# Performance work log

Hardware: AMD Instinct MI355X
Metric: run time of the kernel (lower is better)

Reference implementation:

```python
import jax, jax.numpy as jnp
import numpy as np

WD, WH, WW = 1, 8, 8           # window size
NH = 2                          # num heads
EPS = 1e-5                      # torch LayerNorm default


def _layernorm(x, g, b):
    mu = jnp.mean(x, axis=-1, keepdims=True)
    var = jnp.mean((x - mu) ** 2, axis=-1, keepdims=True)
    return (x - mu) * jax.lax.rsqrt(var + EPS) * g + b


def setup_inputs() -> dict:
    key = jax.random.key(0)
    ks = jax.random.split(key, 12)
    C, H = 192, 768  # dim, mlp hidden
    w = lambda k, shape: (jax.random.normal(k, shape, jnp.float32) * 0.02)
    return {
        "x": jax.random.normal(ks[0], (2, 8, 96, 96, C), jnp.float32),
        "norm3_g": jnp.ones((C,), jnp.float32),
        "norm3_b": jnp.zeros((C,), jnp.float32),
        "in_proj_w": w(ks[1], (3 * C, C)),
        "in_proj_b": jnp.zeros((3 * C,), jnp.float32),
        "out_proj_w": w(ks[2], (C, C)),
        "out_proj_b": jnp.zeros((C,), jnp.float32),
        "norm4_g": jnp.ones((C,), jnp.float32),
        "norm4_b": jnp.zeros((C,), jnp.float32),
        "fc1_w": w(ks[3], (H, C)),
        "fc1_b": jnp.zeros((H,), jnp.float32),
        "fc2_w": w(ks[4], (C, H)),
        "fc2_b": jnp.zeros((C,), jnp.float32),
    }


def _part3(x, norm3_g, norm3_b, in_proj_w, in_proj_b, out_proj_w, out_proj_b):
    B, D, H, W, C = x.shape
    Dn, Hn, Wn = D // WD, H // WH, W // WW
    P = Hn * Wn          # spatial windows
    Wt = WD * WH * WW    # tokens per window (64)
    L = Dn * Wt          # attention sequence length

    xn = _layernorm(x, norm3_g, norm3_b)
    # window partition: (B, Dn, Hn, Wn, wd, wh, ww, C)
    xw = xn.reshape(B, Dn, WD, Hn, WH, Wn, WW, C).transpose(0, 1, 3, 5, 2, 4, 6, 7)
    # tgt: (B, Dn, P, Wt, C) -> h: (B*P, Dn*Wt, C)
    tgt = xw.reshape(B, Dn, P, Wt, C)
    h = tgt.transpose(0, 2, 1, 3, 4).reshape(B * P, L, C)

    # qkv projection (torch Linear convention: x @ W.T + b)
    qkv = h @ in_proj_w.T + in_proj_b          # (Bp, L, 3C)
    q, k, v = jnp.split(qkv, 3, axis=-1)
    hd = C // NH
    q = q.reshape(B * P, L, NH, hd)
    k = k.reshape(B * P, L, NH, hd)
    v = v.reshape(B * P, L, NH, hd)

    # block-causal mask over temporal index (each block is Wt x Wt)
    neg_inf = jnp.finfo(jnp.float32).min
    tmask = jnp.triu(jnp.full((Dn, Dn), neg_inf, jnp.float32), k=1)
    mask = jnp.repeat(jnp.repeat(tmask, Wt, axis=0), Wt, axis=1)  # (L, L)

    scale = 1.0 / np.sqrt(hd)
    scores = jnp.einsum("blhd,bmhd->bhlm", q * scale, k) + mask
    attn = jax.nn.softmax(scores, axis=-1)
    out = jnp.einsum("bhlm,bmhd->blhd", attn, v).reshape(B * P, L, C)
    out = out @ out_proj_w.T + out_proj_b

    # reverse: (B, P, Dn, Wt, C) -> windows -> (B, D, H, W, C)
    out = out.reshape(B, P, Dn, Wt, C).transpose(0, 2, 1, 3, 4)
    out = out.reshape(B, Dn, Hn, Wn, WD, WH, WW, C)
    out = out.transpose(0, 1, 4, 2, 5, 3, 6, 7).reshape(B, D, H, W, C)
    return out


def reference(x, norm3_g, norm3_b, in_proj_w, in_proj_b, out_proj_w, out_proj_b,
              norm4_g, norm4_b, fc1_w, fc1_b, fc2_w, fc2_b):
    x = x + _part3(x, norm3_g, norm3_b, in_proj_w, in_proj_b, out_proj_w, out_proj_b)
    xn = _layernorm(x, norm4_g, norm4_b)
    mlp = jax.nn.gelu(xn @ fc1_w.T + fc1_b, approximate=False) @ fc2_w.T + fc2_b
    return x + mlp
```

## Files before the change

### kernel.cpp

```cpp
#include <hip/hip_runtime.h>
#include <cstdint>
#include <cstddef>


typedef float   f32x4  __attribute__((ext_vector_type(4)));
typedef __bf16  bf16x8 __attribute__((ext_vector_type(8)));
typedef unsigned int   u32x4  __attribute__((ext_vector_type(4)));
typedef unsigned short u16x4  __attribute__((ext_vector_type(4)));

#define DEVI __device__ __forceinline__

DEVI float bf2f(unsigned short u) {
    union { unsigned int i; float f; } v; v.i = ((unsigned int)u) << 16; return v.f;
}
DEVI unsigned short f2bf(float f) {
    unsigned int u = __builtin_bit_cast(unsigned int, f);
    unsigned int r = u + 0x7fffu + ((u >> 16) & 1u);
    return (unsigned short)(r >> 16);
}
DEVI float gelu_fast(float v) {
    float t = v * v;
    float z = v * (1.5957691216057308f + 0.07135481627f * t);
    float e = __expf(z);
    float r = 2.0f / (1.0f + e);
    return v - 0.5f * v * r;
}

typedef __attribute__((address_space(3))) unsigned char       lds_u8;
typedef __attribute__((address_space(1))) const unsigned char g_u8;
DEVI void gl_lds16(const void* g, void* l) {
    __builtin_amdgcn_global_load_lds((g_u8*)g, (lds_u8*)l, 16, 0, 0);
}

__global__ __launch_bounds__(256) void k_wconv(const float* __restrict__ wqkv,
                                               const float* __restrict__ wout,
                                               const float* __restrict__ wfc1,
                                               const float* __restrict__ wfc2,
                                               unsigned short* __restrict__ oq,
                                               unsigned short* __restrict__ oo,
                                               unsigned short* __restrict__ o1,
                                               unsigned short* __restrict__ o2) {
    int i = blockIdx.x * 256 + threadIdx.x;
    if (i < 122880) {
        int r = i / 192;
        oq[i] = (r < 576) ? f2bf(wqkv[i]) : (unsigned short)0;
    } else if (i < 172032) {
        int j = i - 122880; int r = j / 192;
        oo[j] = (r < 192) ? f2bf(wout[j]) : (unsigned short)0;
    } else if (i < 319488) {
        int j = i - 172032;
        o1[j] = f2bf(wfc1[j]);
    } else if (i < 516096) {
        int j = i - 319488; int r = j / 768;
        o2[j] = (r < 192) ? f2bf(wfc2[j]) : (unsigned short)0;
    }
}

__global__ __launch_bounds__(256) void k_ln3(const float* __restrict__ x,
                                             const float* __restrict__ g,
                                             const float* __restrict__ bsh,
                                             unsigned short* __restrict__ h) {
    int w = threadIdx.x >> 6, lane = threadIdx.x & 63;
    int token = blockIdx.x * 4 + w;
    const float* xp = x + (size_t)token * 192;
    float v0 = xp[lane], v1 = xp[lane + 64], v2 = xp[lane + 128];
    float s = v0 + v1 + v2;
#pragma unroll
    for (int off = 32; off; off >>= 1) s += __shfl_xor(s, off);
    float mean = s * (1.f / 192.f);
    float d0 = v0 - mean, d1 = v1 - mean, d2 = v2 - mean;
    float q = d0 * d0 + d1 * d1 + d2 * d2;
#pragma unroll
    for (int off = 32; off; off >>= 1) q += __shfl_xor(q, off);
    float rs = rsqrtf(q * (1.f / 192.f) + 1e-5f);
    int b  = token / (8 * 96 * 96);
    int r0 = token - b * (8 * 96 * 96);
    int d  = r0 / (96 * 96);
    int r1 = r0 - d * (96 * 96);
    int hh = r1 / 96;
    int ww = r1 - hh * 96;
    int bp = b * 144 + (hh >> 3) * 12 + (ww >> 3);
    int l  = d * 64 + (hh & 7) * 8 + (ww & 7);
    unsigned short* hp = h + ((size_t)bp * 512 + l) * 192;
    hp[lane]       = f2bf(d0 * rs * g[lane]       + bsh[lane]);
    hp[lane + 64]  = f2bf(d1 * rs * g[lane + 64]  + bsh[lane + 64]);
    hp[lane + 128] = f2bf(d2 * rs * g[lane + 128] + bsh[lane + 128]);
}

__global__ __launch_bounds__(256) void k_ln4b(const unsigned short* __restrict__ yb,
                                              const float* __restrict__ g,
                                              const float* __restrict__ bsh,
                                              unsigned short* __restrict__ xn) {
    int sub = threadIdx.x >> 5, tl = threadIdx.x & 31;
    size_t row = (size_t)blockIdx.x * 8 + sub;
    const unsigned int* rp = reinterpret_cast<const unsigned int*>(yb + row * 192);
    float v[6];
#pragma unroll
    for (int j = 0; j < 3; j++) {
        unsigned int w = rp[tl + 32 * j];
        v[2 * j]     = bf2f((unsigned short)(w & 0xffffu));
        v[2 * j + 1] = bf2f((unsigned short)(w >> 16));
    }
    float s = v[0] + v[1] + v[2] + v[3] + v[4] + v[5];
#pragma unroll
    for (int off = 1; off < 32; off <<= 1) s += __shfl_xor(s, off);
    float mean = s * (1.f / 192.f);
    float q = 0.f;
#pragma unroll
    for (int j = 0; j < 6; j++) { v[j] -= mean; q += v[j] * v[j]; }
#pragma unroll
    for (int off = 1; off < 32; off <<= 1) q += __shfl_xor(q, off);
    float rs = rsqrtf(q * (1.f / 192.f) + 1e-5f);
    unsigned int* op = reinterpret_cast<unsigned int*>(xn + row * 192);
#pragma unroll
    for (int j = 0; j < 3; j++) {
        int c = (tl + 32 * j) * 2;
        unsigned short lo = f2bf(v[2 * j]     * rs * g[c]     + bsh[c]);
        unsigned short hi = f2bf(v[2 * j + 1] * rs * g[c + 1] + bsh[c + 1]);
        op[tl + 32 * j] = ((unsigned int)hi << 16) | lo;
    }
}

template <int EPI, int K, int NF>
__global__ __launch_bounds__(256) void k_gemm128(const unsigned short* __restrict__ A,
                                                 const unsigned short* __restrict__ Bw,
                                                 const float* __restrict__ bias,
                                                 unsigned short* __restrict__ outb,
                                                 unsigned short* __restrict__ vt,
                                                 float* __restrict__ outf,
                                                 const float* __restrict__ res,
                                                 const unsigned short* __restrict__ resb) {
    constexpr int BN = NF * 32;
    __shared__ unsigned short As[2][128 * 64];
    __shared__ unsigned short Bs[2][BN * 64];
    const int tid = threadIdx.x;
    const int nwg = gridDim.x * gridDim.y;
    const int flat = blockIdx.y * gridDim.x + blockIdx.x;
    const int swz = (flat & 7) * (nwg >> 3) + (flat >> 3);
    const int bx = swz % gridDim.x, by = swz / gridDim.x;
    const int row0 = by * 128, col0 = bx * BN;
    const int wv = tid >> 6, lane = tid & 63, lr = lane & 15, lg = lane >> 4;
    const int wr = wv >> 1, wc = wv & 1;
    const int sr = lane >> 3, sc = lane & 7;
    f32x4 acc[4][NF] = {};

    auto stage = [&](int t, int buf) {
        int k0 = t * 64;
#pragma unroll
        for (int i = 0; i < 4; i++) {
            int gq = wv * 4 + i;
            int r = gq * 8 + sr;
            int j = sc ^ (r & 7);
            gl_lds16(A + (size_t)(row0 + r) * K + k0 + j * 8, &As[buf][gq * 512]);
        }
#pragma unroll
        for (int i = 0; i < NF; i++) {
            int gq = wv * NF + i;
            int r = gq * 8 + sr;
            int j = sc ^ (r & 7);
            gl_lds16(Bw + (size_t)(col0 + r) * K + k0 + j * 8, &Bs[buf][gq * 512]);
        }
    };

    const int NT = K / 64;
    stage(0, 0);
    for (int t = 0; t < NT; ++t) {
        int cur = t & 1;
        if (t + 1 < NT) {
            stage(t + 1, cur ^ 1);
            if constexpr (NF == 4) asm volatile("s_waitcnt vmcnt(8)" ::: "memory");
            else                   asm volatile("s_waitcnt vmcnt(10)" ::: "memory");
        } else {
            asm volatile("s_waitcnt vmcnt(0)" ::: "memory");
        }
        __builtin_amdgcn_sched_barrier(0);
        __builtin_amdgcn_s_barrier();
        __builtin_amdgcn_sched_barrier(0);
#pragma unroll
        for (int kk = 0; kk < 64; kk += 32) {
            bf16x8 af[4], bf[NF];
#pragma unroll
            for (int m = 0; m < 4; m++) {
                int r = wr * 64 + m * 16 + lr;
                int j = ((kk >> 3) + lg) ^ (r & 7);
                af[m] = __builtin_bit_cast(bf16x8,
                    *reinterpret_cast<const u32x4*>(&As[cur][r * 64 + j * 8]));
            }
#pragma unroll
            for (int n = 0; n < NF; n++) {
                int r = wc * (NF * 16) + n * 16 + lr;
                int j = ((kk >> 3) + lg) ^ (r & 7);
                bf[n] = __builtin_bit_cast(bf16x8,
                    *reinterpret_cast<const u32x4*>(&Bs[cur][r * 64 + j * 8]));
            }
#pragma unroll
            for (int m = 0; m < 4; m++)
#pragma unroll
                for (int n = 0; n < NF; n++)
                    acc[m][n] = __builtin_amdgcn_mfma_f32_16x16x32_bf16(bf[n], af[m], acc[m][n], 0, 0, 0);
        }
        __builtin_amdgcn_sched_barrier(0);
        __builtin_amdgcn_s_barrier();
        __builtin_amdgcn_sched_barrier(0);
    }

#pragma unroll
    for (int m = 0; m < 4; m++) {
        const int arow = row0 + wr * 64 + m * 16 + lr;
#pragma unroll
        for (int n = 0; n < NF; n++) {
            const int colb = col0 + wc * (NF * 16) + n * 16 + lg * 4;
            if constexpr (EPI == 0) {
                if (colb < 384) {
                    f32x4 b4 = *reinterpret_cast<const f32x4*>(bias + colb);
                    float sc2 = (colb < 192) ? 0.1020620726159658f : 1.f;
                    u16x4 pk;
#pragma unroll
                    for (int rr = 0; rr < 4; rr++) pk[rr] = f2bf((acc[m][n][rr] + b4[rr]) * sc2);
                    *reinterpret_cast<u16x4*>(outb + (size_t)arow * 384 + colb) = pk;
                } else if (colb < 576) {
                    int head = (colb >= 480) ? 1 : 0;
                    int bp = arow >> 9, tok = arow & 511;
                    size_t vb = ((size_t)(bp * 2 + head) * 96 + (colb - 384 - head * 96)) * 512 + tok;
#pragma unroll
                    for (int rr = 0; rr < 4; rr++)
                        vt[vb + (size_t)rr * 512] = f2bf(acc[m][n][rr] + bias[colb + rr]);
                }
            } else if constexpr (EPI == 1) {
                if (colb < 192) {
                    int bp = arow >> 9, l = arow & 511;
                    int bb = bp / 144, p = bp - bb * 144;
                    int hn = p / 12, wn = p - hn * 12;
                    int dn = l >> 6, t_ = l & 63;
                    size_t tok = ((size_t)((bb * 8 + dn) * 96 + hn * 8 + (t_ >> 3)) * 96 + wn * 8 + (t_ & 7));
                    size_t idx = tok * 192 + colb;
                    f32x4 r4 = *reinterpret_cast<const f32x4*>(res + idx);
                    f32x4 b4 = *reinterpret_cast<const f32x4*>(bias + colb);
                    u16x4 pk;
#pragma unroll
                    for (int rr = 0; rr < 4; rr++) pk[rr] = f2bf(r4[rr] + acc[m][n][rr] + b4[rr]);
                    *reinterpret_cast<u16x4*>(outb + idx) = pk;
                }
            } else if constexpr (EPI == 2) {
                f32x4 b4 = *reinterpret_cast<const f32x4*>(bias + colb);
                u16x4 pk;
#pragma unroll
                for (int rr = 0; rr < 4; rr++) pk[rr] = f2bf(gelu_fast(acc[m][n][rr] + b4[rr]));
                *reinterpret_cast<u16x4*>(outb + (size_t)arow * 768 + colb) = pk;
            } else {
                f32x4 b4 = *reinterpret_cast<const f32x4*>(bias + colb);
                u16x4 rb = *reinterpret_cast<const u16x4*>(resb + (size_t)arow * 192 + colb);
                f32x4 o4;
#pragma unroll
                for (int rr = 0; rr < 4; rr++) o4[rr] = bf2f(rb[rr]) + acc[m][n][rr] + b4[rr];
                *reinterpret_cast<f32x4*>(outf + (size_t)arow * 192 + colb) = o4;
            }
        }
    }
}

__global__ __launch_bounds__(512) void k_attn(const unsigned short* __restrict__ qk,
                                              const unsigned short* __restrict__ vt,
                                              unsigned short* __restrict__ aout) {
    __shared__ unsigned short Ks[64][104];
    __shared__ unsigned short Vs[96][72];
    __shared__ unsigned short Ps[8][16][72];

    int bid = (blockIdx.x & 7) * 288 + (blockIdx.x >> 3);
    int bp = bid >> 3, rest = bid & 7, head = rest >> 2, pr = rest & 3;
    int tid = threadIdx.x, wv = tid >> 6, lane = tid & 63;
    int lr = lane & 15, lg = lane >> 4;
    int wq = wv & 3, wt = wv >> 2;
    int nk = 2 * pr + 2;

    size_t qrow0 = (size_t)bp * 512 + (size_t)(2 * pr + wt) * 64;
    const unsigned short* vbase = vt + (size_t)(bp * 2 + head) * 96 * 512;
    size_t krowb = (size_t)bp * 512;

    bf16x8 qf[3];
    {
        const unsigned short* qp = qk + (qrow0 + wq * 16 + lr) * 384 + head * 96 + lg * 8;
#pragma unroll
        for (int ks = 0; ks < 3; ks++)
            qf[ks] = __builtin_bit_cast(bf16x8, *reinterpret_cast<const u32x4*>(qp + ks * 32));
    }

    f32x4 o[6] = {};
    float m_ = -1e30f, lsum = 0.f;

    u32x4 sreg[3];
    auto issue = [&](int dnk) {
#pragma unroll
        for (int i = 0; i < 3; i++) {
            int c = tid + i * 512;
            if (c < 768) {
                int r = c / 12, cc = c - r * 12;
                sreg[i] = *reinterpret_cast<const u32x4*>(
                    qk + (krowb + dnk * 64 + r) * 384 + 192 + head * 96 + cc * 8);
            } else {
                int c2 = c - 768; int d = c2 >> 3, tb = c2 & 7;
                sreg[i] = *reinterpret_cast<const u32x4*>(
                    vbase + (size_t)d * 512 + dnk * 64 + tb * 8);
            }
        }
    };
    auto commit = [&]() {
#pragma unroll
        for (int i = 0; i < 3; i++) {
            int c = tid + i * 512;
            if (c < 768) {
                int r = c / 12, cc = c - r * 12;
                *reinterpret_cast<u32x4*>(&Ks[r][cc * 8]) = sreg[i];
            } else {
                int c2 = c - 768; int d = c2 >> 3, tb = c2 & 7;
                *reinterpret_cast<u32x4*>(&Vs[d][tb * 8]) = sreg[i];
            }
        }
    };

    issue(0);
    for (int dnk = 0; dnk < nk; ++dnk) {
        commit();
        __syncthreads();
        if (dnk + 1 < nk) issue(dnk + 1);
        if (wt == 1 || dnk < nk - 1) {
            f32x4 st[4] = {};
#pragma unroll
            for (int ks = 0; ks < 3; ks++) {
#pragma unroll
                for (int ct = 0; ct < 4; ct++) {
                    bf16x8 kf = __builtin_bit_cast(bf16x8,
                        *reinterpret_cast<const u32x4*>(&Ks[ct * 16 + lr][ks * 32 + lg * 8]));
                    st[ct] = __builtin_amdgcn_mfma_f32_16x16x32_bf16(kf, qf[ks], st[ct], 0, 0, 0);
                }
            }
            float mx = st[0][0];
#pragma unroll
            for (int ct = 0; ct < 4; ct++)
#pragma unroll
                for (int rr = 0; rr < 4; rr++) mx = fmaxf(mx, st[ct][rr]);
            mx = fmaxf(mx, __shfl_xor(mx, 16));
            mx = fmaxf(mx, __shfl_xor(mx, 32));
            float mnew = fmaxf(m_, mx);
            float corr = __expf(m_ - mnew);
            m_ = mnew;
            float ps = 0.f;
#pragma unroll
            for (int ct = 0; ct < 4; ct++) {
                u16x4 pk;
#pragma unroll
                for (int rr = 0; rr < 4; rr++) {
                    float pv = __expf(st[ct][rr] - mnew);
                    ps += pv;
                    pk[rr] = f2bf(pv);
                }
                *reinterpret_cast<u16x4*>(&Ps[wv][lr][ct * 16 + lg * 4]) = pk;
            }
            ps += __shfl_xor(ps, 16);
            ps += __shfl_xor(ps, 32);
            lsum = lsum * corr + ps;
#pragma unroll
            for (int rr = 0; rr < 4; rr++) {
                float cr = __shfl(corr, (lane & 48) | (lg * 4 + rr));
#pragma unroll
                for (int nf = 0; nf < 6; nf++) o[nf][rr] *= cr;
            }
#pragma unroll
            for (int kk = 0; kk < 2; kk++) {
                bf16x8 pf = __builtin_bit_cast(bf16x8,
                    *reinterpret_cast<const u32x4*>(&Ps[wv][lr][kk * 32 + lg * 8]));
#pragma unroll
                for (int nf = 0; nf < 6; nf++) {
                    bf16x8 vf = __builtin_bit_cast(bf16x8,
                        *reinterpret_cast<const u32x4*>(&Vs[nf * 16 + lr][kk * 32 + lg * 8]));
                    o[nf] = __builtin_amdgcn_mfma_f32_16x16x32_bf16(pf, vf, o[nf], 0, 0, 0);
                }
            }
        }
        __syncthreads();
    }

#pragma unroll
    for (int rr = 0; rr < 4; rr++) {
        float li = __shfl(lsum, (lane & 48) | (lg * 4 + rr));
        float inv = 1.f / li;
        size_t row = qrow0 + wq * 16 + lg * 4 + rr;
#pragma unroll
        for (int nf = 0; nf < 6; nf++)
            aout[row * 192 + head * 96 + nf * 16 + lr] = f2bf(o[nf][rr] * inv);
    }
}

extern "C" void kernel_launch(void* const* d_in, const int* in_sizes, int n_in,
                              void* d_out, int out_size, void* d_ws, size_t ws_size,
                              hipStream_t stream) {
    const float* x    = (const float*)d_in[0];
    const float* n3g  = (const float*)d_in[1];
    const float* n3b  = (const float*)d_in[2];
    const float* wqkv = (const float*)d_in[3];
    const float* bqkv = (const float*)d_in[4];
    const float* wout = (const float*)d_in[5];
    const float* bout = (const float*)d_in[6];
    const float* n4g  = (const float*)d_in[7];
    const float* n4b  = (const float*)d_in[8];
    const float* wfc1 = (const float*)d_in[9];
    const float* bfc1 = (const float*)d_in[10];
    const float* wfc2 = (const float*)d_in[11];
    const float* bfc2 = (const float*)d_in[12];
    float* out = (float*)d_out;

    char* ws = (char*)d_ws;
    unsigned short* qk     = (unsigned short*)(ws + 0);
    unsigned short* vt     = (unsigned short*)(ws + 113246208);
    unsigned short* h      = (unsigned short*)(ws + 169869312);
    unsigned short* attn   = (unsigned short*)(ws + 226492416);
    unsigned short* xn4    = (unsigned short*)(ws + 226492416);
    unsigned short* hidden = (unsigned short*)(ws + 0);
    unsigned short* wq_bf  = (unsigned short*)(ws + 283115520);
    unsigned short* wo_bf  = (unsigned short*)(ws + 283361280);
    unsigned short* w1_bf  = (unsigned short*)(ws + 283459584);
    unsigned short* w2_bf  = (unsigned short*)(ws + 283754496);
    unsigned short* ybf    = (unsigned short*)(ws + 284147712);

    k_wconv<<<2016, 256, 0, stream>>>(wqkv, wout, wfc1, wfc2, wq_bf, wo_bf, w1_bf, w2_bf);
    k_ln3<<<36864, 256, 0, stream>>>(x, n3g, n3b, h);
    k_gemm128<0, 192, 4><<<dim3(5, 1152), 256, 0, stream>>>(h, wq_bf, bqkv, qk, vt, nullptr, nullptr, nullptr);
    k_attn<<<2304, 512, 0, stream>>>(qk, vt, attn);
    k_gemm128<1, 192, 4><<<dim3(2, 1152), 256, 0, stream>>>(attn, wo_bf, bout, ybf, nullptr, nullptr, x, nullptr);
    k_ln4b<<<18432, 256, 0, stream>>>(ybf, n4g, n4b, xn4);
    k_gemm128<2, 192, 4><<<dim3(6, 1152), 256, 0, stream>>>(xn4, w1_bf, bfc1, hidden, nullptr, nullptr, nullptr, nullptr);
    k_gemm128<3, 768, 6><<<dim3(1, 1152), 256, 0, stream>>>(hidden, w2_bf, bfc2, nullptr, nullptr, out, nullptr, ybf);
}
```

Before: 600.5 us.

## Fuse LN4, fc1, GELU and fc2 into one MLP kernel; fold LN affine into weights

```diff
diff --git a/kernel.cpp b/kernel.cpp
--- a/kernel.cpp
+++ b/kernel.cpp
@@ -36,29 +36,49 @@
                                                const float* __restrict__ wout,
                                                const float* __restrict__ wfc1,
                                                const float* __restrict__ wfc2,
+                                               const float* __restrict__ n3g,
+                                               const float* __restrict__ n4g,
                                                unsigned short* __restrict__ oq,
                                                unsigned short* __restrict__ oo,
                                                unsigned short* __restrict__ o1,
                                                unsigned short* __restrict__ o2) {
     int i = blockIdx.x * 256 + threadIdx.x;
     if (i < 122880) {
-        int r = i / 192;
-        oq[i] = (r < 576) ? f2bf(wqkv[i]) : (unsigned short)0;
+        int r = i / 192, c = i - r * 192;
+        oq[i] = (r < 576) ? f2bf(wqkv[i] * n3g[c]) : (unsigned short)0;
     } else if (i < 172032) {
         int j = i - 122880; int r = j / 192;
         oo[j] = (r < 192) ? f2bf(wout[j]) : (unsigned short)0;
     } else if (i < 319488) {
-        int j = i - 172032;
-        o1[j] = f2bf(wfc1[j]);
+        int j = i - 172032; int c = j % 192;
+        o1[j] = f2bf(wfc1[j] * n4g[c]);
     } else if (i < 516096) {
         int j = i - 319488; int r = j / 768;
         o2[j] = (r < 192) ? f2bf(wfc2[j]) : (unsigned short)0;
     }
 }
 
+__global__ __launch_bounds__(256) void k_bias(const float* __restrict__ wqkv,
+                                              const float* __restrict__ bqkv,
+                                              const float* __restrict__ n3b,
+                                              const float* __restrict__ wfc1,
+                                              const float* __restrict__ bfc1,
+                                              const float* __restrict__ n4b,
+                                              float* __restrict__ beffq,
+                                              float* __restrict__ beff1) {
+    int wid = blockIdx.x * 4 + (threadIdx.x >> 6);
+    int lane = threadIdx.x & 63;
+    const float* wrow; const float* bb; float base; float* dst;
+    if (wid < 576) { wrow = wqkv + (size_t)wid * 192; bb = n3b; base = bqkv[wid]; dst = beffq + wid; }
+    else { int h = wid - 576; wrow = wfc1 + (size_t)h * 192; bb = n4b; base = bfc1[h]; dst = beff1 + h; }
+    float s = wrow[lane] * bb[lane] + wrow[lane + 64] * bb[lane + 64]
+            + wrow[lane + 128] * bb[lane + 128];
+#pragma unroll
+    for (int off = 32; off; off >>= 1) s += __shfl_xor(s, off);
+    if (lane == 0) *dst = base + s;
+}
+
 __global__ __launch_bounds__(256) void k_ln3(const float* __restrict__ x,
-                                             const float* __restrict__ g,
-                                             const float* __restrict__ bsh,
                                              unsigned short* __restrict__ h) {
     int w = threadIdx.x >> 6, lane = threadIdx.x & 63;
     int token = blockIdx.x * 4 + w;
@@ -82,43 +102,9 @@
     int bp = b * 144 + (hh >> 3) * 12 + (ww >> 3);
     int l  = d * 64 + (hh & 7) * 8 + (ww & 7);
     unsigned short* hp = h + ((size_t)bp * 512 + l) * 192;
-    hp[lane]       = f2bf(d0 * rs * g[lane]       + bsh[lane]);
-    hp[lane + 64]  = f2bf(d1 * rs * g[lane + 64]  + bsh[lane + 64]);
-    hp[lane + 128] = f2bf(d2 * rs * g[lane + 128] + bsh[lane + 128]);
-}
-
-__global__ __launch_bounds__(256) void k_ln4b(const unsigned short* __restrict__ yb,
-                                              const float* __restrict__ g,
-                                              const float* __restrict__ bsh,
-                                              unsigned short* __restrict__ xn) {
-    int sub = threadIdx.x >> 5, tl = threadIdx.x & 31;
-    size_t row = (size_t)blockIdx.x * 8 + sub;
-    const unsigned int* rp = reinterpret_cast<const unsigned int*>(yb + row * 192);
-    float v[6];
-#pragma unroll
-    for (int j = 0; j < 3; j++) {
-        unsigned int w = rp[tl + 32 * j];
-        v[2 * j]     = bf2f((unsigned short)(w & 0xffffu));
-        v[2 * j + 1] = bf2f((unsigned short)(w >> 16));
-    }
-    float s = v[0] + v[1] + v[2] + v[3] + v[4] + v[5];
-#pragma unroll
-    for (int off = 1; off < 32; off <<= 1) s += __shfl_xor(s, off);
-    float mean = s * (1.f / 192.f);
-    float q = 0.f;
-#pragma unroll
-    for (int j = 0; j < 6; j++) { v[j] -= mean; q += v[j] * v[j]; }
-#pragma unroll
-    for (int off = 1; off < 32; off <<= 1) q += __shfl_xor(q, off);
-    float rs = rsqrtf(q * (1.f / 192.f) + 1e-5f);
-    unsigned int* op = reinterpret_cast<unsigned int*>(xn + row * 192);
-#pragma unroll
-    for (int j = 0; j < 3; j++) {
-        int c = (tl + 32 * j) * 2;
-        unsigned short lo = f2bf(v[2 * j]     * rs * g[c]     + bsh[c]);
-        unsigned short hi = f2bf(v[2 * j + 1] * rs * g[c + 1] + bsh[c + 1]);
-        op[tl + 32 * j] = ((unsigned int)hi << 16) | lo;
-    }
+    hp[lane]       = f2bf(d0 * rs);
+    hp[lane + 64]  = f2bf(d1 * rs);
+    hp[lane + 128] = f2bf(d2 * rs);
 }
 
 template <int EPI, int K, int NF>
@@ -127,18 +113,15 @@
                                                  const float* __restrict__ bias,
                                                  unsigned short* __restrict__ outb,
                                                  unsigned short* __restrict__ vt,
-                                                 float* __restrict__ outf,
-                                                 const float* __restrict__ res,
-                                                 const unsigned short* __restrict__ resb) {
-    constexpr int BN = NF * 32;
+                                                 const float* __restrict__ res) {
     __shared__ unsigned short As[2][128 * 64];
-    __shared__ unsigned short Bs[2][BN * 64];
+    __shared__ unsigned short Bs[2][NF * 32 * 64];
     const int tid = threadIdx.x;
     const int nwg = gridDim.x * gridDim.y;
     const int flat = blockIdx.y * gridDim.x + blockIdx.x;
     const int swz = (flat & 7) * (nwg >> 3) + (flat >> 3);
     const int bx = swz % gridDim.x, by = swz / gridDim.x;
-    const int row0 = by * 128, col0 = bx * BN;
+    const int row0 = by * 128, col0 = bx * (NF * 32);
     const int wv = tid >> 6, lane = tid & 63, lr = lane & 15, lg = lane >> 4;
     const int wr = wv >> 1, wc = wv & 1;
     const int sr = lane >> 3, sc = lane & 7;
@@ -169,7 +152,7 @@
         if (t + 1 < NT) {
             stage(t + 1, cur ^ 1);
             if constexpr (NF == 4) asm volatile("s_waitcnt vmcnt(8)" ::: "memory");
-            else                   asm volatile("s_waitcnt vmcnt(10)" ::: "memory");
+            else                   asm volatile("s_waitcnt vmcnt(7)" ::: "memory");
         } else {
             asm volatile("s_waitcnt vmcnt(0)" ::: "memory");
         }
@@ -207,10 +190,10 @@
 #pragma unroll
     for (int m = 0; m < 4; m++) {
         const int arow = row0 + wr * 64 + m * 16 + lr;
-#pragma unroll
-        for (int n = 0; n < NF; n++) {
-            const int colb = col0 + wc * (NF * 16) + n * 16 + lg * 4;
-            if constexpr (EPI == 0) {
+        if constexpr (EPI == 0) {
+#pragma unroll
+            for (int n = 0; n < NF; n++) {
+                const int colb = col0 + wc * (NF * 16) + n * 16 + lg * 4;
                 if (colb < 384) {
                     f32x4 b4 = *reinterpret_cast<const f32x4*>(bias + colb);
                     float sc2 = (colb < 192) ? 0.1020620726159658f : 1.f;
@@ -226,34 +209,23 @@
                     for (int rr = 0; rr < 4; rr++)
                         vt[vb + (size_t)rr * 512] = f2bf(acc[m][n][rr] + bias[colb + rr]);
                 }
-            } else if constexpr (EPI == 1) {
-                if (colb < 192) {
-                    int bp = arow >> 9, l = arow & 511;
-                    int bb = bp / 144, p = bp - bb * 144;
-                    int hn = p / 12, wn = p - hn * 12;
-                    int dn = l >> 6, t_ = l & 63;
-                    size_t tok = ((size_t)((bb * 8 + dn) * 96 + hn * 8 + (t_ >> 3)) * 96 + wn * 8 + (t_ & 7));
-                    size_t idx = tok * 192 + colb;
-                    f32x4 r4 = *reinterpret_cast<const f32x4*>(res + idx);
-                    f32x4 b4 = *reinterpret_cast<const f32x4*>(bias + colb);
-                    u16x4 pk;
-#pragma unroll
-                    for (int rr = 0; rr < 4; rr++) pk[rr] = f2bf(r4[rr] + acc[m][n][rr] + b4[rr]);
-                    *reinterpret_cast<u16x4*>(outb + idx) = pk;
-                }
-            } else if constexpr (EPI == 2) {
+            }
+        } else {
+            int bp = arow >> 9, l = arow & 511;
+            int bb = bp / 144, p = bp - bb * 144;
+            int hn = p / 12, wn = p - hn * 12;
+            int dn = l >> 6, t_ = l & 63;
+            size_t tok = ((size_t)((bb * 8 + dn) * 96 + hn * 8 + (t_ >> 3)) * 96 + wn * 8 + (t_ & 7));
+#pragma unroll
+            for (int n = 0; n < NF; n++) {
+                const int colb = col0 + wc * (NF * 16) + n * 16 + lg * 4;
+                size_t idx = tok * 192 + colb;
+                f32x4 r4 = *reinterpret_cast<const f32x4*>(res + idx);
                 f32x4 b4 = *reinterpret_cast<const f32x4*>(bias + colb);
                 u16x4 pk;
 #pragma unroll
-                for (int rr = 0; rr < 4; rr++) pk[rr] = f2bf(gelu_fast(acc[m][n][rr] + b4[rr]));
-                *reinterpret_cast<u16x4*>(outb + (size_t)arow * 768 + colb) = pk;
-            } else {
-                f32x4 b4 = *reinterpret_cast<const f32x4*>(bias + colb);
-                u16x4 rb = *reinterpret_cast<const u16x4*>(resb + (size_t)arow * 192 + colb);
-                f32x4 o4;
-#pragma unroll
-                for (int rr = 0; rr < 4; rr++) o4[rr] = bf2f(rb[rr]) + acc[m][n][rr] + b4[rr];
-                *reinterpret_cast<f32x4*>(outf + (size_t)arow * 192 + colb) = o4;
+                for (int rr = 0; rr < 4; rr++) pk[rr] = f2bf(r4[rr] + acc[m][n][rr] + b4[rr]);
+                *reinterpret_cast<u16x4*>(outb + idx) = pk;
             }
         }
     }
@@ -388,6 +360,145 @@
 #pragma unroll
         for (int nf = 0; nf < 6; nf++)
             aout[row * 192 + head * 96 + nf * 16 + lr] = f2bf(o[nf][rr] * inv);
+    }
+}
+
+__global__ __launch_bounds__(256, 4) void k_mlp3(const unsigned short* __restrict__ ybf,
+                                                 const unsigned short* __restrict__ w1,
+                                                 const unsigned short* __restrict__ w2,
+                                                 const float* __restrict__ beff1,
+                                                 const float* __restrict__ b2,
+                                                 float* __restrict__ out) {
+    __shared__ unsigned short XN[3][64][64];
+    __shared__ unsigned short Hs[64][64];
+    const int tid = threadIdx.x;
+    const int bid = (blockIdx.x & 7) * 288 + (blockIdx.x >> 3);
+    const int row0 = bid * 64;
+    const int wv = tid >> 6, lane = tid & 63, lr = lane & 15, lg = lane >> 4;
+    const int tHalf = wv & 1, oH = wv >> 1;
+
+#pragma unroll
+    for (int i = 0; i < 6; i++) {
+        int g = wv * 6 + i;
+        int sub = g >> 3, rg = g & 7;
+        int r = rg * 8 + (lane >> 3);
+        int c = (lane & 7) ^ (r & 7);
+        gl_lds16(ybf + (size_t)(row0 + r) * 192 + sub * 64 + c * 8, &XN[sub][rg * 8][0]);
+    }
+    __syncthreads();
+
+    {
+        int r = tid >> 2, q = tid & 3;
+        float sum = 0.f, ssq = 0.f;
+        u16x4 vv[6][2];
+#pragma unroll
+        for (int ci = 0; ci < 6; ci++) {
+            int c = q * 6 + ci;
+            int j = (c & 7) ^ (r & 7);
+            unsigned short* p8 = &XN[c >> 3][r][j * 8];
+            vv[ci][0] = *reinterpret_cast<u16x4*>(p8);
+            vv[ci][1] = *reinterpret_cast<u16x4*>(p8 + 4);
+#pragma unroll
+            for (int e = 0; e < 4; e++) {
+                float a = bf2f(vv[ci][0][e]), b = bf2f(vv[ci][1][e]);
+                sum += a + b; ssq += a * a + b * b;
+            }
+        }
+        sum += __shfl_xor(sum, 1); ssq += __shfl_xor(ssq, 1);
+        sum += __shfl_xor(sum, 2); ssq += __shfl_xor(ssq, 2);
+        float mu = sum * (1.f / 192.f);
+        float rs = rsqrtf(ssq * (1.f / 192.f) - mu * mu + 1e-5f);
+#pragma unroll
+        for (int ci = 0; ci < 6; ci++) {
+            int c = q * 6 + ci;
+            int j = (c & 7) ^ (r & 7);
+            unsigned short* p8 = &XN[c >> 3][r][j * 8];
+            u16x4 o0, o1;
+#pragma unroll
+            for (int e = 0; e < 4; e++) {
+                o0[e] = f2bf((bf2f(vv[ci][0][e]) - mu) * rs);
+                o1[e] = f2bf((bf2f(vv[ci][1][e]) - mu) * rs);
+            }
+            *reinterpret_cast<u16x4*>(p8) = o0;
+            *reinterpret_cast<u16x4*>(p8 + 4) = o1;
+        }
+    }
+    __syncthreads();
+
+    f32x4 accO[2][6] = {};
+    for (int s = 0; s < 12; ++s) {
+        f32x4 acc1[2][2] = {};
+#pragma unroll
+        for (int kk = 0; kk < 6; kk++) {
+            int sub = kk >> 1;
+            bf16x8 ax[2];
+#pragma unroll
+            for (int m = 0; m < 2; m++) {
+                int t = tHalf * 32 + m * 16 + lr;
+                int j = ((kk & 1) * 4 + lg) ^ (t & 7);
+                ax[m] = __builtin_bit_cast(bf16x8,
+                    *reinterpret_cast<const u32x4*>(&XN[sub][t][j * 8]));
+            }
+#pragma unroll
+            for (int n = 0; n < 2; n++) {
+                bf16x8 bw = __builtin_bit_cast(bf16x8, *reinterpret_cast<const u32x4*>(
+                    w1 + (size_t)(s * 64 + oH * 32 + n * 16 + lr) * 192 + kk * 32 + lg * 8));
+#pragma unroll
+                for (int m = 0; m < 2; m++)
+                    acc1[m][n] = __builtin_amdgcn_mfma_f32_16x16x32_bf16(bw, ax[m], acc1[m][n], 0, 0, 0);
+            }
+        }
+#pragma unroll
+        for (int m = 0; m < 2; m++) {
+            int t = tHalf * 32 + m * 16 + lr;
+#pragma unroll
+            for (int n = 0; n < 2; n++) {
+                int h0 = oH * 32 + n * 16 + lg * 4;
+                f32x4 b4 = *reinterpret_cast<const f32x4*>(beff1 + s * 64 + h0);
+                u16x4 pk;
+#pragma unroll
+                for (int rr = 0; rr < 4; rr++) pk[rr] = f2bf(gelu_fast(acc1[m][n][rr] + b4[rr]));
+                int jw = (h0 >> 3) ^ (t & 7);
+                *reinterpret_cast<u16x4*>(&Hs[t][jw * 8 + (h0 & 7)]) = pk;
+            }
+        }
+        __syncthreads();
+
+#pragma unroll
+        for (int kk = 0; kk < 2; kk++) {
+            bf16x8 ah[2];
+#pragma unroll
+            for (int m = 0; m < 2; m++) {
+                int t = tHalf * 32 + m * 16 + lr;
+                int j = (kk * 4 + lg) ^ (t & 7);
+                ah[m] = __builtin_bit_cast(bf16x8,
+                    *reinterpret_cast<const u32x4*>(&Hs[t][j * 8]));
+            }
+#pragma unroll
+            for (int n = 0; n < 6; n++) {
+                bf16x8 bw = __builtin_bit_cast(bf16x8, *reinterpret_cast<const u32x4*>(
+                    w2 + (size_t)(oH * 96 + n * 16 + lr) * 768 + s * 64 + kk * 32 + lg * 8));
+#pragma unroll
+                for (int m = 0; m < 2; m++)
+                    accO[m][n] = __builtin_amdgcn_mfma_f32_16x16x32_bf16(bw, ah[m], accO[m][n], 0, 0, 0);
+            }
+        }
+        __syncthreads();
+    }
+
+#pragma unroll
+    for (int m = 0; m < 2; m++) {
+        int t = row0 + tHalf * 32 + m * 16 + lr;
+#pragma unroll
+        for (int n = 0; n < 6; n++) {
+            int o0 = oH * 96 + n * 16 + lg * 4;
+            f32x4 b4 = *reinterpret_cast<const f32x4*>(b2 + o0);
+            u16x4 rb = *reinterpret_cast<const u16x4*>(ybf + (size_t)t * 192 + o0);
+            f32x4 o4;
+#pragma unroll
+            for (int rr = 0; rr < 4; rr++) o4[rr] = bf2f(rb[rr]) + accO[m][n][rr] + b4[rr];
+            *reinterpret_cast<f32x4*>(out + (size_t)t * 192 + o0) = o4;
+        }
     }
 }
 
@@ -410,24 +521,23 @@
     float* out = (float*)d_out;
 
     char* ws = (char*)d_ws;
-    unsigned short* qk     = (unsigned short*)(ws + 0);
-    unsigned short* vt     = (unsigned short*)(ws + 113246208);
-    unsigned short* h      = (unsigned short*)(ws + 169869312);
-    unsigned short* attn   = (unsigned short*)(ws + 226492416);
-    unsigned short* xn4    = (unsigned short*)(ws + 226492416);
-    unsigned short* hidden = (unsigned short*)(ws + 0);
-    unsigned short* wq_bf  = (unsigned short*)(ws + 283115520);
-    unsigned short* wo_bf  = (unsigned short*)(ws + 283361280);
-    unsigned short* w1_bf  = (unsigned short*)(ws + 283459584);
-    unsigned short* w2_bf  = (unsigned short*)(ws + 283754496);
-    unsigned short* ybf    = (unsigned short*)(ws + 284147712);
-
-    k_wconv<<<2016, 256, 0, stream>>>(wqkv, wout, wfc1, wfc2, wq_bf, wo_bf, w1_bf, w2_bf);
-    k_ln3<<<36864, 256, 0, stream>>>(x, n3g, n3b, h);
-    k_gemm128<0, 192, 4><<<dim3(5, 1152), 256, 0, stream>>>(h, wq_bf, bqkv, qk, vt, nullptr, nullptr, nullptr);
+    unsigned short* qk    = (unsigned short*)(ws + 0);
+    unsigned short* vt    = (unsigned short*)(ws + 113246208);
+    unsigned short* attn  = (unsigned short*)(ws + 169869312);
+    unsigned short* ybf   = (unsigned short*)(ws + 226492416);
+    unsigned short* h     = (unsigned short*)(ws + 283115520);
+    unsigned short* wq_bf = (unsigned short*)(ws + 339738624);
+    unsigned short* wo_bf = (unsigned short*)(ws + 339984384);
+    unsigned short* w1_bf = (unsigned short*)(ws + 340082688);
+    unsigned short* w2_bf = (unsigned short*)(ws + 340377600);
+    float*          beffq = (float*)(ws + 340770816);
+    float*          beff1 = (float*)(ws + 340773120);
+
+    k_wconv<<<2016, 256, 0, stream>>>(wqkv, wout, wfc1, wfc2, n3g, n4g, wq_bf, wo_bf, w1_bf, w2_bf);
+    k_bias<<<336, 256, 0, stream>>>(wqkv, bqkv, n3b, wfc1, bfc1, n4b, beffq, beff1);
+    k_ln3<<<36864, 256, 0, stream>>>(x, h);
+    k_gemm128<0, 192, 4><<<dim3(5, 1152), 256, 0, stream>>>(h, wq_bf, beffq, qk, vt, nullptr);
     k_attn<<<2304, 512, 0, stream>>>(qk, vt, attn);
-    k_gemm128<1, 192, 4><<<dim3(2, 1152), 256, 0, stream>>>(attn, wo_bf, bout, ybf, nullptr, nullptr, x, nullptr);
-    k_ln4b<<<18432, 256, 0, stream>>>(ybf, n4g, n4b, xn4);
-    k_gemm128<2, 192, 4><<<dim3(6, 1152), 256, 0, stream>>>(xn4, w1_bf, bfc1, hidden, nullptr, nullptr, nullptr, nullptr);
-    k_gemm128<3, 768, 6><<<dim3(1, 1152), 256, 0, stream>>>(hidden, w2_bf, bfc2, nullptr, nullptr, out, nullptr, ybf);
-}
+    k_gemm128<1, 192, 3><<<dim3(2, 1152), 256, 0, stream>>>(attn, wo_bf, bout, ybf, nullptr, x);
+    k_mlp3<<<2304, 256, 0, stream>>>(ybf, w1_bf, w2_bf, beff1, bfc2, out);
+}
```

Measured after the change: 671.9 us. 1.12x slower.

## Fold LayerNorm affine into GEMM weights and retile out-proj and fc2 GEMMs

Applied to the files above, without the earlier changes.

```diff
diff --git a/kernel.cpp b/kernel.cpp
--- a/kernel.cpp
+++ b/kernel.cpp
@@ -36,29 +36,49 @@
                                                const float* __restrict__ wout,
                                                const float* __restrict__ wfc1,
                                                const float* __restrict__ wfc2,
+                                               const float* __restrict__ n3g,
+                                               const float* __restrict__ n4g,
                                                unsigned short* __restrict__ oq,
                                                unsigned short* __restrict__ oo,
                                                unsigned short* __restrict__ o1,
                                                unsigned short* __restrict__ o2) {
     int i = blockIdx.x * 256 + threadIdx.x;
     if (i < 122880) {
-        int r = i / 192;
-        oq[i] = (r < 576) ? f2bf(wqkv[i]) : (unsigned short)0;
+        int r = i / 192, c = i - r * 192;
+        oq[i] = (r < 576) ? f2bf(wqkv[i] * n3g[c]) : (unsigned short)0;
     } else if (i < 172032) {
         int j = i - 122880; int r = j / 192;
         oo[j] = (r < 192) ? f2bf(wout[j]) : (unsigned short)0;
     } else if (i < 319488) {
-        int j = i - 172032;
-        o1[j] = f2bf(wfc1[j]);
+        int j = i - 172032; int c = j % 192;
+        o1[j] = f2bf(wfc1[j] * n4g[c]);
     } else if (i < 516096) {
         int j = i - 319488; int r = j / 768;
         o2[j] = (r < 192) ? f2bf(wfc2[j]) : (unsigned short)0;
     }
 }
 
+__global__ __launch_bounds__(256) void k_bias(const float* __restrict__ wqkv,
+                                              const float* __restrict__ bqkv,
+                                              const float* __restrict__ n3b,
+                                              const float* __restrict__ wfc1,
+                                              const float* __restrict__ bfc1,
+                                              const float* __restrict__ n4b,
+                                              float* __restrict__ beffq,
+                                              float* __restrict__ beff1) {
+    int wid = blockIdx.x * 4 + (threadIdx.x >> 6);
+    int lane = threadIdx.x & 63;
+    const float* wrow; const float* bb; float base; float* dst;
+    if (wid < 576) { wrow = wqkv + (size_t)wid * 192; bb = n3b; base = bqkv[wid]; dst = beffq + wid; }
+    else { int h = wid - 576; wrow = wfc1 + (size_t)h * 192; bb = n4b; base = bfc1[h]; dst = beff1 + h; }
+    float s = wrow[lane] * bb[lane] + wrow[lane + 64] * bb[lane + 64]
+            + wrow[lane + 128] * bb[lane + 128];
+#pragma unroll
+    for (int off = 32; off; off >>= 1) s += __shfl_xor(s, off);
+    if (lane == 0) *dst = base + s;
+}
+
 __global__ __launch_bounds__(256) void k_ln3(const float* __restrict__ x,
-                                             const float* __restrict__ g,
-                                             const float* __restrict__ bsh,
                                              unsigned short* __restrict__ h) {
     int w = threadIdx.x >> 6, lane = threadIdx.x & 63;
     int token = blockIdx.x * 4 + w;
@@ -82,14 +102,12 @@
     int bp = b * 144 + (hh >> 3) * 12 + (ww >> 3);
     int l  = d * 64 + (hh & 7) * 8 + (ww & 7);
     unsigned short* hp = h + ((size_t)bp * 512 + l) * 192;
-    hp[lane]       = f2bf(d0 * rs * g[lane]       + bsh[lane]);
-    hp[lane + 64]  = f2bf(d1 * rs * g[lane + 64]  + bsh[lane + 64]);
-    hp[lane + 128] = f2bf(d2 * rs * g[lane + 128] + bsh[lane + 128]);
+    hp[lane]       = f2bf(d0 * rs);
+    hp[lane + 64]  = f2bf(d1 * rs);
+    hp[lane + 128] = f2bf(d2 * rs);
 }
 
 __global__ __launch_bounds__(256) void k_ln4b(const unsigned short* __restrict__ yb,
-                                              const float* __restrict__ g,
-                                              const float* __restrict__ bsh,
                                               unsigned short* __restrict__ xn) {
     int sub = threadIdx.x >> 5, tl = threadIdx.x & 31;
     size_t row = (size_t)blockIdx.x * 8 + sub;
@@ -114,9 +132,8 @@
     unsigned int* op = reinterpret_cast<unsigned int*>(xn + row * 192);
 #pragma unroll
     for (int j = 0; j < 3; j++) {
-        int c = (tl + 32 * j) * 2;
-        unsigned short lo = f2bf(v[2 * j]     * rs * g[c]     + bsh[c]);
-        unsigned short hi = f2bf(v[2 * j + 1] * rs * g[c + 1] + bsh[c + 1]);
+        unsigned short lo = f2bf(v[2 * j]     * rs);
+        unsigned short hi = f2bf(v[2 * j + 1] * rs);
         op[tl + 32 * j] = ((unsigned int)hi << 16) | lo;
     }
 }
@@ -127,18 +144,17 @@
                                                  const float* __restrict__ bias,
                                                  unsigned short* __restrict__ outb,
                                                  unsigned short* __restrict__ vt,
-                                                 float* __restrict__ outf,
                                                  const float* __restrict__ res,
-                                                 const unsigned short* __restrict__ resb) {
-    constexpr int BN = NF * 32;
+                                                 const unsigned short* __restrict__ resb,
+                                                 float* __restrict__ outf) {
     __shared__ unsigned short As[2][128 * 64];
-    __shared__ unsigned short Bs[2][BN * 64];
+    __shared__ unsigned short Bs[2][NF * 32 * 64];
     const int tid = threadIdx.x;
     const int nwg = gridDim.x * gridDim.y;
     const int flat = blockIdx.y * gridDim.x + blockIdx.x;
     const int swz = (flat & 7) * (nwg >> 3) + (flat >> 3);
     const int bx = swz % gridDim.x, by = swz / gridDim.x;
-    const int row0 = by * 128, col0 = bx * BN;
+    const int row0 = by * 128, col0 = bx * (NF * 32);
     const int wv = tid >> 6, lane = tid & 63, lr = lane & 15, lg = lane >> 4;
     const int wr = wv >> 1, wc = wv & 1;
     const int sr = lane >> 3, sc = lane & 7;
@@ -169,7 +185,7 @@
         if (t + 1 < NT) {
             stage(t + 1, cur ^ 1);
             if constexpr (NF == 4) asm volatile("s_waitcnt vmcnt(8)" ::: "memory");
-            else                   asm volatile("s_waitcnt vmcnt(10)" ::: "memory");
+            else                   asm volatile("s_waitcnt vmcnt(7)" ::: "memory");
         } else {
             asm volatile("s_waitcnt vmcnt(0)" ::: "memory");
         }
@@ -207,10 +223,10 @@
 #pragma unroll
     for (int m = 0; m < 4; m++) {
         const int arow = row0 + wr * 64 + m * 16 + lr;
-#pragma unroll
-        for (int n = 0; n < NF; n++) {
-            const int colb = col0 + wc * (NF * 16) + n * 16 + lg * 4;
-            if constexpr (EPI == 0) {
+        if constexpr (EPI == 0) {
+#pragma unroll
+            for (int n = 0; n < NF; n++) {
+                const int colb = col0 + wc * (NF * 16) + n * 16 + lg * 4;
                 if (colb < 384) {
                     f32x4 b4 = *reinterpret_cast<const f32x4*>(bias + colb);
                     float sc2 = (colb < 192) ? 0.1020620726159658f : 1.f;
@@ -226,34 +242,45 @@
                     for (int rr = 0; rr < 4; rr++)
                         vt[vb + (size_t)rr * 512] = f2bf(acc[m][n][rr] + bias[colb + rr]);
                 }
-            } else if constexpr (EPI == 1) {
-                if (colb < 192) {
-                    int bp = arow >> 9, l = arow & 511;
-                    int bb = bp / 144, p = bp - bb * 144;
-                    int hn = p / 12, wn = p - hn * 12;
-                    int dn = l >> 6, t_ = l & 63;
-                    size_t tok = ((size_t)((bb * 8 + dn) * 96 + hn * 8 + (t_ >> 3)) * 96 + wn * 8 + (t_ & 7));
-                    size_t idx = tok * 192 + colb;
-                    f32x4 r4 = *reinterpret_cast<const f32x4*>(res + idx);
-                    f32x4 b4 = *reinterpret_cast<const f32x4*>(bias + colb);
-                    u16x4 pk;
-#pragma unroll
-                    for (int rr = 0; rr < 4; rr++) pk[rr] = f2bf(r4[rr] + acc[m][n][rr] + b4[rr]);
-                    *reinterpret_cast<u16x4*>(outb + idx) = pk;
-                }
-            } else if constexpr (EPI == 2) {
+            }
+        } else if constexpr (EPI == 1) {
+            int bp = arow >> 9, l = arow & 511;
+            int bb = bp / 144, p = bp - bb * 144;
+            int hn = p / 12, wn = p - hn * 12;
+            int dn = l >> 6, t_ = l & 63;
+            size_t tok = ((size_t)((bb * 8 + dn) * 96 + hn * 8 + (t_ >> 3)) * 96 + wn * 8 + (t_ & 7));
+#pragma unroll
+            for (int n = 0; n < NF; n++) {
+                const int colb = col0 + wc * (NF * 16) + n * 16 + lg * 4;
+                size_t idx = tok * 192 + colb;
+                f32x4 r4 = *reinterpret_cast<const f32x4*>(res + idx);
                 f32x4 b4 = *reinterpret_cast<const f32x4*>(bias + colb);
                 u16x4 pk;
 #pragma unroll
+                for (int rr = 0; rr < 4; rr++) pk[rr] = f2bf(r4[rr] + acc[m][n][rr] + b4[rr]);
+                *reinterpret_cast<u16x4*>(outb + idx) = pk;
+            }
+        } else if constexpr (EPI == 2) {
+#pragma unroll
+            for (int n = 0; n < NF; n++) {
+                const int colb = col0 + wc * (NF * 16) + n * 16 + lg * 4;
+                f32x4 b4 = *reinterpret_cast<const f32x4*>(bias + colb);
+                u16x4 pk;
+#pragma unroll
                 for (int rr = 0; rr < 4; rr++) pk[rr] = f2bf(gelu_fast(acc[m][n][rr] + b4[rr]));
                 *reinterpret_cast<u16x4*>(outb + (size_t)arow * 768 + colb) = pk;
-            } else {
+            }
+        } else {
+#pragma unroll
+            for (int n = 0; n < NF; n++) {
+                const int colb = col0 + wc * (NF * 16) + n * 16 + lg * 4;
+                size_t idx = (size_t)arow * 192 + colb;
                 f32x4 b4 = *reinterpret_cast<const f32x4*>(bias + colb);
-                u16x4 rb = *reinterpret_cast<const u16x4*>(resb + (size_t)arow * 192 + colb);
+                u16x4 rb = *reinterpret_cast<const u16x4*>(resb + idx);
                 f32x4 o4;
 #pragma unroll
                 for (int rr = 0; rr < 4; rr++) o4[rr] = bf2f(rb[rr]) + acc[m][n][rr] + b4[rr];
-                *reinterpret_cast<f32x4*>(outf + (size_t)arow * 192 + colb) = o4;
+                *reinterpret_cast<f32x4*>(outf + idx) = o4;
             }
         }
     }
@@ -412,22 +439,25 @@
     char* ws = (char*)d_ws;
     unsigned short* qk     = (unsigned short*)(ws + 0);
     unsigned short* vt     = (unsigned short*)(ws + 113246208);
-    unsigned short* h      = (unsigned short*)(ws + 169869312);
-    unsigned short* attn   = (unsigned short*)(ws + 226492416);
-    unsigned short* xn4    = (unsigned short*)(ws + 226492416);
+    unsigned short* attn   = (unsigned short*)(ws + 169869312);
     unsigned short* hidden = (unsigned short*)(ws + 0);
-    unsigned short* wq_bf  = (unsigned short*)(ws + 283115520);
-    unsigned short* wo_bf  = (unsigned short*)(ws + 283361280);
-    unsigned short* w1_bf  = (unsigned short*)(ws + 283459584);
-    unsigned short* w2_bf  = (unsigned short*)(ws + 283754496);
-    unsigned short* ybf    = (unsigned short*)(ws + 284147712);
-
-    k_wconv<<<2016, 256, 0, stream>>>(wqkv, wout, wfc1, wfc2, wq_bf, wo_bf, w1_bf, w2_bf);
-    k_ln3<<<36864, 256, 0, stream>>>(x, n3g, n3b, h);
-    k_gemm128<0, 192, 4><<<dim3(5, 1152), 256, 0, stream>>>(h, wq_bf, bqkv, qk, vt, nullptr, nullptr, nullptr);
+    unsigned short* ybf    = (unsigned short*)(ws + 226492416);
+    unsigned short* h      = (unsigned short*)(ws + 283115520);
+    unsigned short* xn4    = (unsigned short*)(ws + 283115520);
+    unsigned short* wq_bf  = (unsigned short*)(ws + 339738624);
+    unsigned short* wo_bf  = (unsigned short*)(ws + 339984384);
+    unsigned short* w1_bf  = (unsigned short*)(ws + 340082688);
+    unsigned short* w2_bf  = (unsigned short*)(ws + 340377600);
+    float*          beffq  = (float*)(ws + 340770816);
+    float*          beff1  = (float*)(ws + 340773120);
+
+    k_wconv<<<2016, 256, 0, stream>>>(wqkv, wout, wfc1, wfc2, n3g, n4g, wq_bf, wo_bf, w1_bf, w2_bf);
+    k_bias<<<336, 256, 0, stream>>>(wqkv, bqkv, n3b, wfc1, bfc1, n4b, beffq, beff1);
+    k_ln3<<<36864, 256, 0, stream>>>(x, h);
+    k_gemm128<0, 192, 4><<<dim3(5, 1152), 256, 0, stream>>>(h, wq_bf, beffq, qk, vt, nullptr, nullptr, nullptr);
     k_attn<<<2304, 512, 0, stream>>>(qk, vt, attn);
-    k_gemm128<1, 192, 4><<<dim3(2, 1152), 256, 0, stream>>>(attn, wo_bf, bout, ybf, nullptr, nullptr, x, nullptr);
-    k_ln4b<<<18432, 256, 0, stream>>>(ybf, n4g, n4b, xn4);
-    k_gemm128<2, 192, 4><<<dim3(6, 1152), 256, 0, stream>>>(xn4, w1_bf, bfc1, hidden, nullptr, nullptr, nullptr, nullptr);
-    k_gemm128<3, 768, 6><<<dim3(1, 1152), 256, 0, stream>>>(hidden, w2_bf, bfc2, nullptr, nullptr, out, nullptr, ybf);
-}
+    k_gemm128<1, 192, 3><<<dim3(2, 1152), 256, 0, stream>>>(attn, wo_bf, bout, ybf, nullptr, x, nullptr, nullptr);
+    k_ln4b<<<18432, 256, 0, stream>>>(ybf, xn4);
+    k_gemm128<2, 192, 4><<<dim3(6, 1152), 256, 0, stream>>>(xn4, w1_bf, beff1, hidden, nullptr, nullptr, nullptr, nullptr);
+    k_gemm128<3, 768, 3><<<dim3(2, 1152), 256, 0, stream>>>(hidden, w2_bf, bfc2, nullptr, nullptr, nullptr, ybf, out);
+}
```

New measurement: 551.4 us. -8.2%, faster.
